# Kernel optimization log

Measured on AMD Instinct MI355X. Metric: run time of the kernel, lower is better.

Reference implementation:

```python
import jax, jax.numpy as jnp
import numpy as np

B = 8192      # batch
E = 16        # n_experts
D = 128       # per-expert input dim (equal for all experts)
U = 256       # units
F = 256       # feature_dim (gating input)
G = 4         # n_gates
K = 6         # hard-coded top-k in the original call()
TEMP = 0.01   # hard-coded softmax temperature
LEAKY_SLOPE = 0.2  # keras leaky_relu default negative slope


def setup_inputs() -> dict:
    key = jax.random.key(0)
    ks = jax.random.split(key, 5)
    return {
        "inputs": jax.random.normal(ks[0], (B, E * D), dtype=jnp.float32),
        "feature_input": jax.random.normal(ks[1], (B, F), dtype=jnp.float32),
        # stacked per-expert kernels (equal dims -> one [E, D, U] tensor)
        "expert_kernels": jax.random.normal(ks[2], (E, D, U), dtype=jnp.float32) * 0.05,
        "expert_biases": jnp.zeros((E, U), dtype=jnp.float32),
        "gating_kernels": jax.random.normal(ks[3], (G, F, E), dtype=jnp.float32) * 0.1,
        "gating_biases": jnp.zeros((G, E), dtype=jnp.float32),
        "global_weights": jnp.ones((E,), dtype=jnp.float32),
    }


def reference(inputs, feature_input, expert_kernels, expert_biases,
              gating_kernels, gating_biases, global_weights):
    # ---- per-expert dense + bias + LeakyReLU (tf.split loop -> batched einsum) ----
    x = inputs.reshape(B, E, D)                                   # [B, E, D]
    eo = jnp.einsum('bed,edu->bue', x, expert_kernels)            # [B, U, E]
    eo = eo + expert_biases.T[None, :, :]                         # bias per expert
    expert_outputs = jax.nn.leaky_relu(eo, LEAKY_SLOPE)           # [B, U, E]

    # ---- gating: dense + bias + ReLU, scaled by global_weights ----
    g = jnp.einsum('bf,gfe->bge', feature_input, gating_kernels)  # [B, G, E]
    g = jax.nn.relu(g + gating_biases[None, :, :]) * global_weights

    # sharp softmax over experts, then top-k selection
    p = jax.nn.softmax(g / TEMP, axis=-1)                         # [B, G, E]
    top_v, top_i = jax.lax.top_k(p, K)                            # [B, G, K]

    # gather selected expert outputs: [B, G, U, K]
    sel = jnp.take_along_axis(expert_outputs[:, None, :, :],
                              top_i[:, :, None, :], axis=-1)

    # renormalize top-k values with another sharp softmax, weighted combine
    w = jax.nn.softmax(top_v / TEMP, axis=-1)                     # [B, G, K]
    out = jnp.einsum('bguk,bgk->bgu', sel, w)                     # [B, G, U]
    concat_output = out.reshape(B, G * U)                         # concat over gates
    return concat_output, expert_outputs
```

## Files before the change

### kernel.cpp

```cpp
#include <hip/hip_runtime.h>
#include <stdint.h>

#define NB 8192
#define NE 16
#define ND 128
#define NU 256
#define NF 256
#define NG 4
#define NK 6
#define ITEMP_LOG2E 144.26950408889634f

typedef short short4v __attribute__((ext_vector_type(4)));
typedef short short8v __attribute__((ext_vector_type(8)));
typedef float float4v __attribute__((ext_vector_type(4)));

__device__ __forceinline__ short f2bf(float x) {
  uint32_t u = __builtin_bit_cast(uint32_t, x);
  u += 0x7FFFu + ((u >> 16) & 1u);
  return (short)(u >> 16);
}

__global__ __launch_bounds__(256) void prep_kernel(
    const float* __restrict__ ek,
    const float* __restrict__ feat,
    const float* __restrict__ gk,
    const float* __restrict__ gbias,
    const float* __restrict__ gw,
    short* __restrict__ pb,
    float* __restrict__ wd)
{
  __shared__ float fsh[32 * 256];
  int bid = blockIdx.x, tid = threadIdx.x;
  if (bid < 256) {
    int gid = (bid << 8) | tid;
    int lane = gid & 63, ut = (gid >> 6) & 15, ks = (gid >> 10) & 3, e = gid >> 12;
    int krow = ks * 32 + ((lane >> 4) * 8);
    int ucol = ut * 16 + (lane & 15);
    const float* src = ek + (size_t)(e * 128 + krow) * 256 + ucol;
    short8v v;
#pragma unroll
    for (int j = 0; j < 8; ++j) v[j] = f2bf(src[(size_t)j * 256]);
    *(short8v*)(pb + (size_t)gid * 8) = v;
  } else {
    int b0 = (bid - 256) * 32;
    {
      const float4v* s = (const float4v*)(feat + (size_t)b0 * 256);
      float4v* d = (float4v*)fsh;
      for (int i = tid; i < 2048; i += 256) d[i] = __builtin_nontemporal_load(s + i);
    }
    __syncthreads();
    int w = tid >> 6, lane = tid & 63;
    int gate = lane >> 4, e = lane & 15;
    float gwv = gw[e];
    float bias = gbias[gate * 16 + e];
    float acc[8];
#pragma unroll
    for (int i = 0; i < 8; ++i) acc[i] = bias;
    const float* gkp = gk + (size_t)gate * (NF * NE) + e;
    for (int f = 0; f < NF; f += 4) {
      float g0 = gkp[(f + 0) * 16], g1 = gkp[(f + 1) * 16];
      float g2 = gkp[(f + 2) * 16], g3 = gkp[(f + 3) * 16];
#pragma unroll
      for (int i = 0; i < 8; ++i) {
        float4v fv = *(const float4v*)&fsh[(w * 8 + i) * 256 + f];
        acc[i] = fmaf(fv[0], g0, acc[i]);
        acc[i] = fmaf(fv[1], g1, acc[i]);
        acc[i] = fmaf(fv[2], g2, acc[i]);
        acc[i] = fmaf(fv[3], g3, acc[i]);
      }
    }
#pragma unroll 1
    for (int i = 0; i < 8; ++i) {
      int b = b0 + w * 8 + i;
      float v = acc[i] > 0.f ? acc[i] : 0.f;
      v *= gwv;
      float m = v;
#pragma unroll
      for (int off = 1; off < 16; off <<= 1) m = fmaxf(m, __shfl_xor(m, off, 16));
      float ex = exp2f((v - m) * ITEMP_LOG2E);
      float s = ex;
#pragma unroll
      for (int off = 1; off < 16; off <<= 1) s += __shfl_xor(s, off, 16);
      float p = ex / s;
      float cur = p;
      float topv[NK]; int topi[NK];
#pragma unroll
      for (int r = 0; r < NK; ++r) {
        float mv = cur;
#pragma unroll
        for (int off = 1; off < 16; off <<= 1) mv = fmaxf(mv, __shfl_xor(mv, off, 16));
        int cand = (cur == mv) ? e : 16;
#pragma unroll
        for (int off = 1; off < 16; off <<= 1) cand = min(cand, __shfl_xor(cand, off, 16));
        topv[r] = mv; topi[r] = cand;
        if (e == cand) cur = -1.f;
      }
      float wv[NK], wsum = 0.f;
#pragma unroll
      for (int r = 0; r < NK; ++r) {
        wv[r] = exp2f((topv[r] - topv[0]) * ITEMP_LOG2E);
        wsum += wv[r];
      }
      float inv = 1.f / wsum;
      float wdv = 0.f;
#pragma unroll
      for (int r = 0; r < NK; ++r) wdv = (topi[r] == e) ? wv[r] * inv : wdv;
      wd[(size_t)b * 64 + gate * 16 + e] = wdv;
    }
  }
}

#define APITCH 2056
#define WPITCH 64

__global__ __launch_bounds__(512, 2) void moe_kernel(
    const float* __restrict__ x,
    const float* __restrict__ eb,
    const short* __restrict__ pb,
    const float* __restrict__ wd,
    float* __restrict__ out)
{
  __shared__ __align__(16) short ash[32 * APITCH];
  __shared__ __align__(16) float wsh[32 * WPITCH];
  __shared__ __align__(16) float stg[8 * 512];
  int bt = blockIdx.x, tid = threadIdx.x;
#pragma unroll
  for (int k = 0; k < 4; ++k) {
    int i = tid + k * 512;
    wsh[(i >> 6) * WPITCH + (i & 63)] = wd[(size_t)bt * 2048 + i];
  }
  {
    const float4v* s = (const float4v*)(x + (size_t)bt * 32 * 2048);
#pragma unroll
    for (int it = 0; it < 32; ++it) {
      int idx = tid + it * 512;
      int row = idx >> 9;
      int colf = (idx & 511) << 2;
      float4v v = __builtin_nontemporal_load(s + idx);
      short4v sv;
      sv[0] = f2bf(v[0]); sv[1] = f2bf(v[1]); sv[2] = f2bf(v[2]); sv[3] = f2bf(v[3]);
      *(short4v*)&ash[row * APITCH + colf] = sv;
    }
  }
  __syncthreads();

  int w = tid >> 6, lane = tid & 63;
  int btile = w >> 2, utq = w & 3;
  int q = lane >> 4, col = lane & 15;
  int am = lane & 15;
  float* outcat = out;
  float* outeo = out + (size_t)NB * NG * NU;
  const short8v* pbv = (const short8v*)pb;
  float* ws = stg + w * 512;
  size_t bb = (size_t)bt * 32 + btile * 16;
  int arow = (btile * 16 + am) * APITCH;
  int wrow = (btile * 16 + q * 4) * WPITCH;

  float csave[4][4];

#pragma unroll 2
  for (int t = 0; t < 4; ++t) {
    int ut = utq * 4 + t;
    float4v acc[16];
    float4v zero = {0.f, 0.f, 0.f, 0.f};
#pragma unroll
    for (int e = 0; e < 16; ++e) acc[e] = zero;
#pragma unroll
    for (int e = 0; e < 16; ++e) {
#pragma unroll
      for (int ks = 0; ks < 4; ++ks) {
        short8v a = *(const short8v*)&ash[arow + e * 128 + ks * 32 + q * 8];
        short8v b = pbv[((e * 4 + ks) * 16 + ut) * 64 + lane];
        acc[e] = __builtin_amdgcn_mfma_f32_16x16x32_bf16(a, b, acc[e], 0, 0, 0);
      }
    }
    float v[16][4];
#pragma unroll
    for (int e = 0; e < 16; ++e) {
      float bv = eb[e * 256 + ut * 16 + col];
#pragma unroll
      for (int r = 0; r < 4; ++r) {
        float z = acc[e][r] + bv;
        v[e][r] = z > 0.f ? z : 0.2f * z;
      }
    }
#pragma unroll
    for (int r = 0; r < 4; ++r) {
#pragma unroll
      for (int round = 0; round < 2; ++round) {
        if ((q >> 1) == round) {
          float* base = ws + (q & 1) * 256 + col * 16;
#pragma unroll
          for (int c = 0; c < 4; ++c) {
            float4v o = {v[4 * c + 0][r], v[4 * c + 1][r], v[4 * c + 2][r], v[4 * c + 3][r]};
            *(float4v*)(base + ((c ^ (col & 3)) * 4)) = o;
          }
        }
        __builtin_amdgcn_wave_barrier();
#pragma unroll
        for (int h = 0; h < 2; ++h) {
          size_t b = bb + (size_t)((round * 2 + h) * 4 + r);
          float4v val = *(const float4v*)(ws + h * 256 + lane * 4);
          int cc = (lane & 3) ^ ((lane >> 2) & 3);
          float* dst = outeo + b * 4096 + (size_t)ut * 256 + (lane >> 2) * 16 + cc * 4;
          __builtin_nontemporal_store(val, (float4v*)dst);
        }
        __builtin_amdgcn_wave_barrier();
      }
    }
#pragma unroll
    for (int r = 0; r < 4; ++r) {
      size_t b = bb + (size_t)(q * 4 + r);
#pragma unroll
      for (int g = 0; g < 4; ++g) {
        float sacc = 0.f;
#pragma unroll
        for (int ec = 0; ec < 16; ec += 4) {
          float4v wv = *(const float4v*)&wsh[wrow + r * WPITCH + g * 16 + ec];
          sacc = fmaf(wv[0], v[ec][r], sacc);
          sacc = fmaf(wv[1], v[ec + 1][r], sacc);
          sacc = fmaf(wv[2], v[ec + 2][r], sacc);
          sacc = fmaf(wv[3], v[ec + 3][r], sacc);
        }
        if ((t & 1) == 0) {
          csave[r][g] = sacc;
        } else {
          float* cb = outcat + b * 1024 + g * 256 + (ut - 1) * 16 + col;
          __builtin_nontemporal_store(csave[r][g], cb);
          __builtin_nontemporal_store(sacc, cb + 16);
        }
      }
    }
  }
}

extern "C" void kernel_launch(void* const* d_in, const int* in_sizes, int n_in,
                              void* d_out, int out_size, void* d_ws, size_t ws_size,
                              hipStream_t stream) {
  const float* x     = (const float*)d_in[0];
  const float* feat  = (const float*)d_in[1];
  const float* ek    = (const float*)d_in[2];
  const float* eb    = (const float*)d_in[3];
  const float* gk    = (const float*)d_in[4];
  const float* gbias = (const float*)d_in[5];
  const float* gw    = (const float*)d_in[6];
  float* out = (float*)d_out;
  float* wd  = (float*)d_ws;
  short* pbf = (short*)((char*)d_ws + (size_t)NB * NG * NE * 4);

  prep_kernel<<<512, 256, 0, stream>>>(ek, feat, gk, gbias, gw, pbf, wd);
  moe_kernel<<<256, 512, 0, stream>>>(x, eb, pbf, wd, out);
}
```

Baseline: 371.0 us.

## Fuse gating/top-k into MoE kernel and split work across 16 waves

Moves the gating dense, softmax and top-k computation out of the prep kernel and into the main MoE kernel. Two waves compute the routing weights straight into shared memory while the other fourteen load and convert the activation tile, which removes the workspace round-trip for the weights. The block grows to 1024 threads, and each wave now handles two unit tiles instead of four. The staging layout for the expert-output transpose is simplified, and the nontemporal output stores are replaced with regular stores. Risks include lower occupancy with 1024-thread blocks and large shared memory, more register pressure, and the gating waves reading features directly from global memory.

```diff
diff --git a/kernel.cpp b/kernel.cpp
--- a/kernel.cpp
+++ b/kernel.cpp
@@ -22,118 +22,41 @@
 
 __global__ __launch_bounds__(256) void prep_kernel(
     const float* __restrict__ ek,
+    short* __restrict__ pb)
+{
+  int gid = (blockIdx.x << 8) | threadIdx.x;
+  int lane = gid & 63, ut = (gid >> 6) & 15, ks = (gid >> 10) & 3, e = gid >> 12;
+  int krow = ks * 32 + ((lane >> 4) * 8);
+  int ucol = ut * 16 + (lane & 15);
+  const float* src = ek + (size_t)(e * 128 + krow) * 256 + ucol;
+  short8v v;
+#pragma unroll
+  for (int j = 0; j < 8; ++j) v[j] = f2bf(src[(size_t)j * 256]);
+  *(short8v*)(pb + (size_t)gid * 8) = v;
+}
+
+#define APITCH 2056
+#define WPITCH 64
+
+__global__ __launch_bounds__(1024, 4) void moe_kernel(
+    const float* __restrict__ x,
     const float* __restrict__ feat,
     const float* __restrict__ gk,
     const float* __restrict__ gbias,
     const float* __restrict__ gw,
-    short* __restrict__ pb,
-    float* __restrict__ wd)
-{
-  __shared__ float fsh[32 * 256];
-  int bid = blockIdx.x, tid = threadIdx.x;
-  if (bid < 256) {
-    int gid = (bid << 8) | tid;
-    int lane = gid & 63, ut = (gid >> 6) & 15, ks = (gid >> 10) & 3, e = gid >> 12;
-    int krow = ks * 32 + ((lane >> 4) * 8);
-    int ucol = ut * 16 + (lane & 15);
-    const float* src = ek + (size_t)(e * 128 + krow) * 256 + ucol;
-    short8v v;
-#pragma unroll
-    for (int j = 0; j < 8; ++j) v[j] = f2bf(src[(size_t)j * 256]);
-    *(short8v*)(pb + (size_t)gid * 8) = v;
-  } else {
-    int b0 = (bid - 256) * 32;
-    {
-      const float4v* s = (const float4v*)(feat + (size_t)b0 * 256);
-      float4v* d = (float4v*)fsh;
-      for (int i = tid; i < 2048; i += 256) d[i] = __builtin_nontemporal_load(s + i);
-    }
-    __syncthreads();
-    int w = tid >> 6, lane = tid & 63;
-    int gate = lane >> 4, e = lane & 15;
-    float gwv = gw[e];
-    float bias = gbias[gate * 16 + e];
-    float acc[8];
-#pragma unroll
-    for (int i = 0; i < 8; ++i) acc[i] = bias;
-    const float* gkp = gk + (size_t)gate * (NF * NE) + e;
-    for (int f = 0; f < NF; f += 4) {
-      float g0 = gkp[(f + 0) * 16], g1 = gkp[(f + 1) * 16];
-      float g2 = gkp[(f + 2) * 16], g3 = gkp[(f + 3) * 16];
-#pragma unroll
-      for (int i = 0; i < 8; ++i) {
-        float4v fv = *(const float4v*)&fsh[(w * 8 + i) * 256 + f];
-        acc[i] = fmaf(fv[0], g0, acc[i]);
-        acc[i] = fmaf(fv[1], g1, acc[i]);
-        acc[i] = fmaf(fv[2], g2, acc[i]);
-        acc[i] = fmaf(fv[3], g3, acc[i]);
-      }
-    }
-#pragma unroll 1
-    for (int i = 0; i < 8; ++i) {
-      int b = b0 + w * 8 + i;
-      float v = acc[i] > 0.f ? acc[i] : 0.f;
-      v *= gwv;
-      float m = v;
-#pragma unroll
-      for (int off = 1; off < 16; off <<= 1) m = fmaxf(m, __shfl_xor(m, off, 16));
-      float ex = exp2f((v - m) * ITEMP_LOG2E);
-      float s = ex;
-#pragma unroll
-      for (int off = 1; off < 16; off <<= 1) s += __shfl_xor(s, off, 16);
-      float p = ex / s;
-      float cur = p;
-      float topv[NK]; int topi[NK];
-#pragma unroll
-      for (int r = 0; r < NK; ++r) {
-        float mv = cur;
-#pragma unroll
-        for (int off = 1; off < 16; off <<= 1) mv = fmaxf(mv, __shfl_xor(mv, off, 16));
-        int cand = (cur == mv) ? e : 16;
-#pragma unroll
-        for (int off = 1; off < 16; off <<= 1) cand = min(cand, __shfl_xor(cand, off, 16));
-        topv[r] = mv; topi[r] = cand;
-        if (e == cand) cur = -1.f;
-      }
-      float wv[NK], wsum = 0.f;
-#pragma unroll
-      for (int r = 0; r < NK; ++r) {
-        wv[r] = exp2f((topv[r] - topv[0]) * ITEMP_LOG2E);
-        wsum += wv[r];
-      }
-      float inv = 1.f / wsum;
-      float wdv = 0.f;
-#pragma unroll
-      for (int r = 0; r < NK; ++r) wdv = (topi[r] == e) ? wv[r] * inv : wdv;
-      wd[(size_t)b * 64 + gate * 16 + e] = wdv;
-    }
-  }
-}
-
-#define APITCH 2056
-#define WPITCH 64
-
-__global__ __launch_bounds__(512, 2) void moe_kernel(
-    const float* __restrict__ x,
     const float* __restrict__ eb,
     const short* __restrict__ pb,
-    const float* __restrict__ wd,
     float* __restrict__ out)
 {
   __shared__ __align__(16) short ash[32 * APITCH];
   __shared__ __align__(16) float wsh[32 * WPITCH];
-  __shared__ __align__(16) float stg[8 * 512];
+  __shared__ __align__(16) float stg[16 * 256];
   int bt = blockIdx.x, tid = threadIdx.x;
-#pragma unroll
-  for (int k = 0; k < 4; ++k) {
-    int i = tid + k * 512;
-    wsh[(i >> 6) * WPITCH + (i & 63)] = wd[(size_t)bt * 2048 + i];
-  }
-  {
+  int w = tid >> 6, lane = tid & 63;
+
+  if (w < 14) {
     const float4v* s = (const float4v*)(x + (size_t)bt * 32 * 2048);
-#pragma unroll
-    for (int it = 0; it < 32; ++it) {
-      int idx = tid + it * 512;
+    for (int idx = w * 64 + lane; idx < 16384; idx += 896) {
       int row = idx >> 9;
       int colf = (idx & 511) << 2;
       float4v v = __builtin_nontemporal_load(s + idx);
@@ -141,25 +64,87 @@
       sv[0] = f2bf(v[0]); sv[1] = f2bf(v[1]); sv[2] = f2bf(v[2]); sv[3] = f2bf(v[3]);
       *(short4v*)&ash[row * APITCH + colf] = sv;
     }
+  } else {
+    int rb = (w - 14) * 16;
+    int gate = lane >> 4, e = lane & 15;
+    float gwv = gw[e];
+    float bias = gbias[gate * 16 + e];
+    const float* gkp = gk + (size_t)gate * (NF * NE) + e;
+#pragma unroll 1
+    for (int p = 0; p < 2; ++p) {
+      float acc[8];
+#pragma unroll
+      for (int i = 0; i < 8; ++i) acc[i] = bias;
+      const float* fb = feat + ((size_t)bt * 32 + rb + p * 8) * 256;
+      for (int f = 0; f < NF; f += 4) {
+        float g0 = gkp[(f + 0) * 16], g1 = gkp[(f + 1) * 16];
+        float g2 = gkp[(f + 2) * 16], g3 = gkp[(f + 3) * 16];
+#pragma unroll
+        for (int i = 0; i < 8; ++i) {
+          float4v fv = *(const float4v*)(fb + i * 256 + f);
+          acc[i] = fmaf(fv[0], g0, acc[i]);
+          acc[i] = fmaf(fv[1], g1, acc[i]);
+          acc[i] = fmaf(fv[2], g2, acc[i]);
+          acc[i] = fmaf(fv[3], g3, acc[i]);
+        }
+      }
+#pragma unroll 1
+      for (int i = 0; i < 8; ++i) {
+        float v = acc[i] > 0.f ? acc[i] : 0.f;
+        v *= gwv;
+        float m = v;
+#pragma unroll
+        for (int off = 1; off < 16; off <<= 1) m = fmaxf(m, __shfl_xor(m, off, 16));
+        float ex = exp2f((v - m) * ITEMP_LOG2E);
+        float s = ex;
+#pragma unroll
+        for (int off = 1; off < 16; off <<= 1) s += __shfl_xor(s, off, 16);
+        float pr = ex / s;
+        float cur = pr;
+        float topv[NK]; int topi[NK];
+#pragma unroll
+        for (int r = 0; r < NK; ++r) {
+          float mv = cur;
+#pragma unroll
+          for (int off = 1; off < 16; off <<= 1) mv = fmaxf(mv, __shfl_xor(mv, off, 16));
+          int cand = (cur == mv) ? e : 16;
+#pragma unroll
+          for (int off = 1; off < 16; off <<= 1) cand = min(cand, __shfl_xor(cand, off, 16));
+          topv[r] = mv; topi[r] = cand;
+          if (e == cand) cur = -1.f;
+        }
+        float wv[NK], wsum = 0.f;
+#pragma unroll
+        for (int r = 0; r < NK; ++r) {
+          wv[r] = exp2f((topv[r] - topv[0]) * ITEMP_LOG2E);
+          wsum += wv[r];
+        }
+        float inv = 1.f / wsum;
+        float wdv = 0.f;
+#pragma unroll
+        for (int r = 0; r < NK; ++r) wdv = (topi[r] == e) ? wv[r] * inv : wdv;
+        wsh[(rb + p * 8 + i) * WPITCH + lane] = wdv;
+      }
+    }
   }
   __syncthreads();
 
-  int w = tid >> 6, lane = tid & 63;
-  int btile = w >> 2, utq = w & 3;
+  int btile = w >> 3, utq = (w >> 1) & 3, th = w & 1;
   int q = lane >> 4, col = lane & 15;
   int am = lane & 15;
   float* outcat = out;
   float* outeo = out + (size_t)NB * NG * NU;
   const short8v* pbv = (const short8v*)pb;
-  float* ws = stg + w * 512;
+  float* ws = stg + w * 256;
   size_t bb = (size_t)bt * 32 + btile * 16;
   int arow = (btile * 16 + am) * APITCH;
   int wrow = (btile * 16 + q * 4) * WPITCH;
 
   float csave[4][4];
 
-#pragma unroll 2
-  for (int t = 0; t < 4; ++t) {
+#pragma unroll 1
+  for (int tl = 0; tl < 2; ++tl) {
+    int t = th * 2 + tl;
     int ut = utq * 4 + t;
     float4v acc[16];
     float4v zero = {0.f, 0.f, 0.f, 0.f};
@@ -187,23 +172,20 @@
 #pragma unroll
     for (int r = 0; r < 4; ++r) {
 #pragma unroll
-      for (int round = 0; round < 2; ++round) {
-        if ((q >> 1) == round) {
-          float* base = ws + (q & 1) * 256 + col * 16;
+      for (int qq = 0; qq < 4; ++qq) {
+        if (q == qq) {
 #pragma unroll
           for (int c = 0; c < 4; ++c) {
             float4v o = {v[4 * c + 0][r], v[4 * c + 1][r], v[4 * c + 2][r], v[4 * c + 3][r]};
-            *(float4v*)(base + ((c ^ (col & 3)) * 4)) = o;
+            *(float4v*)(ws + (c * 16 + col) * 4) = o;
           }
         }
         __builtin_amdgcn_wave_barrier();
-#pragma unroll
-        for (int h = 0; h < 2; ++h) {
-          size_t b = bb + (size_t)((round * 2 + h) * 4 + r);
-          float4v val = *(const float4v*)(ws + h * 256 + lane * 4);
-          int cc = (lane & 3) ^ ((lane >> 2) & 3);
-          float* dst = outeo + b * 4096 + (size_t)ut * 256 + (lane >> 2) * 16 + cc * 4;
-          __builtin_nontemporal_store(val, (float4v*)dst);
+        {
+          size_t b = bb + (size_t)(qq * 4 + r);
+          float4v val = *(const float4v*)(ws + lane * 4);
+          float* dst = outeo + b * 4096 + (size_t)ut * 256 + (lane & 15) * 16 + (lane >> 4) * 4;
+          *(float4v*)dst = val;
         }
         __builtin_amdgcn_wave_barrier();
       }
@@ -222,12 +204,12 @@
           sacc = fmaf(wv[2], v[ec + 2][r], sacc);
           sacc = fmaf(wv[3], v[ec + 3][r], sacc);
         }
-        if ((t & 1) == 0) {
+        if (tl == 0) {
           csave[r][g] = sacc;
         } else {
           float* cb = outcat + b * 1024 + g * 256 + (ut - 1) * 16 + col;
-          __builtin_nontemporal_store(csave[r][g], cb);
-          __builtin_nontemporal_store(sacc, cb + 16);
+          cb[0] = csave[r][g];
+          cb[16] = sacc;
         }
       }
     }
@@ -245,9 +227,8 @@
   const float* gbias = (const float*)d_in[5];
   const float* gw    = (const float*)d_in[6];
   float* out = (float*)d_out;
-  float* wd  = (float*)d_ws;
-  short* pbf = (short*)((char*)d_ws + (size_t)NB * NG * NE * 4);
-
-  prep_kernel<<<512, 256, 0, stream>>>(ek, feat, gk, gbias, gw, pbf, wd);
-  moe_kernel<<<256, 512, 0, stream>>>(x, eb, pbf, wd, out);
-}
+  short* pbf = (short*)d_ws;
+
+  prep_kernel<<<256, 256, 0, stream>>>(ek, pbf);
+  moe_kernel<<<256, 1024, 0, stream>>>(x, feat, gk, gbias, gw, eb, pbf, out);
+}
```

Result: faster. 325.3 us (-12.3%).
